# Kernel tuning notes

Hardware: AMD Instinct MI355X
Metric: run time of the kernel (lower is better)

The kernel has to match this reference:

```python
import jax, jax.numpy as jnp
import numpy as np

N = 20000      # nodes
E = 320000     # edges (before self-loops)
G = 64         # graphs in batch
H = 4          # attention heads
C = 64         # channels per head
HID = H * C    # 256
IN = 128       # input feature dim
LAT = 64       # latent dim
NEG = 0.2      # LeakyReLU negative slope (PyG GATConv default)
BN_EPS = 1e-5
N_LAYERS = 3


def setup_inputs() -> dict:
    key = jax.random.key(0)
    ks = jax.random.split(key, 24)
    s = 0.1
    return dict(
        x=jax.random.normal(ks[0], (N, IN), jnp.float32),
        edge_index=jax.random.randint(ks[1], (2, E), 0, N, dtype=jnp.int32),
        batch=jnp.sort(jax.random.randint(ks[2], (N,), 0, G, dtype=jnp.int32)),
        W0=jax.random.normal(ks[3], (IN, HID), jnp.float32) * s,
        W_rest=jax.random.normal(ks[4], (N_LAYERS - 1, HID, HID), jnp.float32) * s,
        att_src=jax.random.normal(ks[5], (N_LAYERS, H, C), jnp.float32) * s,
        att_dst=jax.random.normal(ks[6], (N_LAYERS, H, C), jnp.float32) * s,
        bias_conv=jax.random.normal(ks[7], (N_LAYERS, HID), jnp.float32) * s,
        bn_gamma=jax.random.uniform(ks[8], (N_LAYERS, HID), jnp.float32) + 0.5,
        bn_beta=jax.random.normal(ks[9], (N_LAYERS, HID), jnp.float32) * s,
        bn_mean=jax.random.normal(ks[10], (N_LAYERS, HID), jnp.float32) * s,
        bn_var=jax.random.uniform(ks[11], (N_LAYERS, HID), jnp.float32) + 0.5,
        lbn_gamma=jax.random.uniform(ks[12], (HID,), jnp.float32) + 0.5,
        lbn_beta=jax.random.normal(ks[13], (HID,), jnp.float32) * s,
        lbn_mean=jax.random.normal(ks[14], (HID,), jnp.float32) * s,
        lbn_var=jax.random.uniform(ks[15], (HID,), jnp.float32) + 0.5,
        fc_W=jax.random.normal(ks[16], (HID, LAT), jnp.float32) * s,
        fc_b=jax.random.normal(ks[17], (LAT,), jnp.float32) * s,
    )


def _gat_layer(x, src, dst, W, a_src, a_dst, bias):
    # linear transform -> [N, H, C]
    xp = (x @ W).reshape(N, H, C)
    # per-node attention scalars [N, H]
    al_s = (xp * a_src).sum(-1)
    al_d = (xp * a_dst).sum(-1)
    # per-edge logit for edge j->i: leaky_relu(a_s[j] + a_d[i])
    e = jax.nn.leaky_relu(al_s[src] + al_d[dst], NEG)  # [E', H]
    # softmax over incoming edges of each target node
    emax = jax.ops.segment_max(e, dst, num_segments=N)  # [N, H]
    ex = jnp.exp(e - emax[dst])
    denom = jax.ops.segment_sum(ex, dst, num_segments=N)
    alpha = ex / (denom[dst] + 1e-16)
    # weighted scatter-add of source features
    msg = xp[src] * alpha[:, :, None]                    # [E', H, C]
    out = jax.ops.segment_sum(msg, dst, num_segments=N)  # [N, H, C]
    return out.reshape(N, HID) + bias


def _bn_eval(x, gamma, beta, mean, var):
    return (x - mean) * jax.lax.rsqrt(var + BN_EPS) * gamma + beta


def reference(x, edge_index, batch, W0, W_rest, att_src, att_dst, bias_conv,
              bn_gamma, bn_beta, bn_mean, bn_var,
              lbn_gamma, lbn_beta, lbn_mean, lbn_var, fc_W, fc_b):
    # PyG convention: edge_index[0]=source, edge_index[1]=target; GATConv adds self-loops
    loop = jnp.arange(N, dtype=edge_index.dtype)
    src = jnp.concatenate([edge_index[0], loop])
    dst = jnp.concatenate([edge_index[1], loop])
    h = x
    for i in range(N_LAYERS):
        W = W0 if i == 0 else W_rest[i - 1]
        h = _gat_layer(h, src, dst, W, att_src[i], att_dst[i], bias_conv[i])
        h = _bn_eval(h, bn_gamma[i], bn_beta[i], bn_mean[i], bn_var[i])
        h = jax.nn.relu(h)
        # dropout is identity in eval mode
    pooled = jax.ops.segment_sum(h, batch, num_segments=G)  # [G, HID]
    pooled = _bn_eval(pooled, lbn_gamma, lbn_beta, lbn_mean, lbn_var)
    return pooled @ fc_W + fc_b  # [G, LAT]
```

## Files before the change

### kernel.cpp

```cpp
#include <hip/hip_runtime.h>
#include <hip/hip_bf16.h>
#include <cmath>

#define NN   20000
#define NE   320000
#define EE   (NE + NN)
#define NG   64
#define NH   4
#define NC   64
#define HIDD 256
#define IND  128
#define LATD 64
#define NEGS 0.2f
#define BNEPS 1e-5f
#define MPAD 20096
#define PSPLIT 16

#define BM 128
#define BN 64
#define BK 64

typedef __attribute__((ext_vector_type(8))) short short8;
typedef __attribute__((ext_vector_type(4))) float f32x4;

__device__ inline int lower_bound_i(const int* __restrict__ b, int n, int key) {
    int lo = 0, hi = n;
    while (lo < hi) { int mid = (lo + hi) >> 1; if (b[mid] < key) lo = mid + 1; else hi = mid; }
    return lo;
}

__device__ inline float sel4(float4 v, int h) {
    float r = v.x;
    r = (h == 1) ? v.y : r;
    r = (h == 2) ? v.z : r;
    r = (h == 3) ? v.w : r;
    return r;
}

__device__ inline float bf2f(unsigned short u) {
    return __uint_as_float(((unsigned int)u) << 16);
}

__global__ void k_cast_x(const float* __restrict__ x, __hip_bfloat16* __restrict__ hbx) {
    int i = blockIdx.x * blockDim.x + threadIdx.x;
    if (i >= NN * IND / 4) return;
    float4 v = ((const float4*)x)[i];
    union { __hip_bfloat16 b[4]; ushort4 u; } cv;
    cv.b[0] = __float2bfloat16(v.x); cv.b[1] = __float2bfloat16(v.y);
    cv.b[2] = __float2bfloat16(v.z); cv.b[3] = __float2bfloat16(v.w);
    ((ushort4*)hbx)[i] = cv.u;
}

__global__ void k_cast_wt(const float* __restrict__ W, int K, __hip_bfloat16* __restrict__ Wt) {
    int k = blockIdx.x;
    int n = threadIdx.x;
    Wt[(size_t)n * K + k] = __float2bfloat16(W[(size_t)k * HIDD + n]);
}

__global__ void k_hist(const int* __restrict__ ei, int* __restrict__ deg) {
    int e = blockIdx.x * blockDim.x + threadIdx.x;
    if (e >= EE) return;
    int d = (e < NE) ? ei[NE + e] : (e - NE);
    atomicAdd(&deg[d], 1);
}

#define SCHUNK ((NN + 255) / 256)
__global__ __launch_bounds__(256) void k_scan256(const int* __restrict__ deg,
                                                 int* __restrict__ row_ptr,
                                                 int* __restrict__ cursor) {
    __shared__ int part[256];
    int tid = threadIdx.x;
    int base = tid * SCHUNK;
    int cnt = NN - base; cnt = cnt < 0 ? 0 : (cnt > SCHUNK ? SCHUNK : cnt);
    int sum = 0;
    for (int j = 0; j < cnt; ++j) sum += deg[base + j];
    part[tid] = sum;
    __syncthreads();
    for (int off = 1; off < 256; off <<= 1) {
        int t = (tid >= off) ? part[tid - off] : 0;
        __syncthreads();
        part[tid] += t;
        __syncthreads();
    }
    int excl = part[tid] - sum;
    for (int j = 0; j < cnt; ++j) {
        row_ptr[base + j] = excl; cursor[base + j] = excl;
        excl += deg[base + j];
    }
    if (tid == 255) row_ptr[NN] = part[255];
}

__global__ void k_csr_scatter(const int* __restrict__ ei, int* __restrict__ cursor,
                              int* __restrict__ col_idx) {
    int e = blockIdx.x * blockDim.x + threadIdx.x;
    if (e >= EE) return;
    int s, d;
    if (e < NE) { s = ei[e]; d = ei[NE + e]; } else { s = d = e - NE; }
    int pos = atomicAdd(&cursor[d], 1);
    col_idx[pos] = s;
}

__global__ __launch_bounds__(256) void k_gemm(const short* __restrict__ A,
                                              const short* __restrict__ Bt,
                                              int K, float* __restrict__ C) {
    __shared__ char As[BM * BK * 2];
    __shared__ char Bs[BN * BK * 2];
    int tid = threadIdx.x;
    int lane = tid & 63;
    int wid = tid >> 6;
    int wm = wid >> 1, wn = wid & 1;
    int bm0 = blockIdx.x * BM, bn0 = blockIdx.y * BN;
    int r16 = lane & 15, kg = lane >> 4;

    f32x4 acc[4][2];
    #pragma unroll
    for (int m = 0; m < 4; ++m)
        #pragma unroll
        for (int n = 0; n < 2; ++n) acc[m][n] = (f32x4){0.f, 0.f, 0.f, 0.f};

    for (int k0 = 0; k0 < K; k0 += BK) {
        __syncthreads();
        #pragma unroll
        for (int p = 0; p < 4; ++p) {
            int row = p * 32 + (tid >> 3);
            int cg  = tid & 7;
            uint4 v = *(const uint4*)(A + (size_t)(bm0 + row) * K + k0 + cg * 8);
            *(uint4*)(As + row * 128 + ((cg * 16) ^ ((row & 7) << 4))) = v;
        }
        #pragma unroll
        for (int p = 0; p < 2; ++p) {
            int row = p * 32 + (tid >> 3);
            int cg  = tid & 7;
            uint4 v = *(const uint4*)(Bt + (size_t)(bn0 + row) * K + k0 + cg * 8);
            *(uint4*)(Bs + row * 128 + ((cg * 16) ^ ((row & 7) << 4))) = v;
        }
        __syncthreads();
        #pragma unroll
        for (int kk = 0; kk < 2; ++kk) {
            short8 af[4], bfr[2];
            int kb = (kk * 32 + kg * 8) * 2;
            #pragma unroll
            for (int m = 0; m < 4; ++m) {
                int row = wm * 64 + m * 16 + r16;
                af[m] = *(const short8*)(As + row * 128 + (kb ^ ((row & 7) << 4)));
            }
            #pragma unroll
            for (int n = 0; n < 2; ++n) {
                int row = wn * 32 + n * 16 + r16;
                bfr[n] = *(const short8*)(Bs + row * 128 + (kb ^ ((row & 7) << 4)));
            }
            #pragma unroll
            for (int m = 0; m < 4; ++m)
                #pragma unroll
                for (int n = 0; n < 2; ++n)
                    acc[m][n] = __builtin_amdgcn_mfma_f32_16x16x32_bf16(af[m], bfr[n], acc[m][n], 0, 0, 0);
        }
    }
    #pragma unroll
    for (int m = 0; m < 4; ++m) {
        int row = bm0 + wm * 64 + m * 16 + kg * 4;
        #pragma unroll
        for (int n = 0; n < 2; ++n) {
            int col = bn0 + wn * 32 + n * 16 + r16;
            #pragma unroll
            for (int r = 0; r < 4; ++r)
                C[(size_t)(row + r) * HIDD + col] = acc[m][n][r];
        }
    }
}

__global__ __launch_bounds__(256) void k_att2(const float* __restrict__ xp,
                                              const float* __restrict__ a_src,
                                              const float* __restrict__ a_dst,
                                              float* __restrict__ al_s,
                                              float* __restrict__ al_d,
                                              __hip_bfloat16* __restrict__ xpb) {
    int wid = threadIdx.x >> 6, lane = threadIdx.x & 63;
    int node = blockIdx.x * 4 + wid;
    if (node >= NN) return;
    int hh = lane >> 4, sub = lane & 15;
    float4 v = ((const float4*)(xp + (size_t)node * HIDD))[lane];
    union { __hip_bfloat16 b[4]; ushort4 u; } cv;
    cv.b[0] = __float2bfloat16(v.x); cv.b[1] = __float2bfloat16(v.y);
    cv.b[2] = __float2bfloat16(v.z); cv.b[3] = __float2bfloat16(v.w);
    ((ushort4*)(xpb + (size_t)node * HIDD))[lane] = cv.u;

    float4 ws = ((const float4*)a_src)[lane];
    float4 wd = ((const float4*)a_dst)[lane];
    float s = v.x * ws.x + v.y * ws.y + v.z * ws.z + v.w * ws.w;
    float d = v.x * wd.x + v.y * wd.y + v.z * wd.z + v.w * wd.w;
    #pragma unroll
    for (int m = 1; m < 16; m <<= 1) {
        s += __shfl_xor(s, m, 64);
        d += __shfl_xor(d, m, 64);
    }
    if (sub == 0) {
        al_s[node * NH + hh] = s;
        al_d[node * NH + hh] = d;
    }
}

__global__ __launch_bounds__(256) void k_gat_agg(
        const int* __restrict__ row_ptr, const int* __restrict__ col_idx,
        const float* __restrict__ al_s, const float* __restrict__ al_d,
        const __hip_bfloat16* __restrict__ xpb,
        const float* __restrict__ bias, const float* __restrict__ bg,
        const float* __restrict__ bb, const float* __restrict__ bm,
        const float* __restrict__ bv,
        float* __restrict__ h, __hip_bfloat16* __restrict__ hb, int wmask) {
    int wid = threadIdx.x >> 6, lane = threadIdx.x & 63;
    int node = blockIdx.x * 4 + wid;
    if (node >= NN) return;
    int lo = row_ptr[node], hi = row_ptr[node + 1];
    int hsel = lane >> 4;
    float adh = sel4(((const float4*)al_d)[node], hsel);

    float4 acc0 = {0,0,0,0}, acc1 = {0,0,0,0}, acc2 = {0,0,0,0}, acc3 = {0,0,0,0};
    float den0 = 0.f, den1 = 0.f, den2 = 0.f, den3 = 0.f;

    int e = lo;
    for (; e + 3 < hi; e += 4) {
        int sc0 = col_idx[e], sc1 = col_idx[e + 1], sc2 = col_idx[e + 2], sc3 = col_idx[e + 3];
        float as0 = al_s[sc0 * NH + hsel];
        float as1 = al_s[sc1 * NH + hsel];
        float as2 = al_s[sc2 * NH + hsel];
        float as3 = al_s[sc3 * NH + hsel];
        ushort4 xv0 = ((const ushort4*)(xpb + (size_t)sc0 * HIDD))[lane];
        ushort4 xv1 = ((const ushort4*)(xpb + (size_t)sc1 * HIDD))[lane];
        ushort4 xv2 = ((const ushort4*)(xpb + (size_t)sc2 * HIDD))[lane];
        ushort4 xv3 = ((const ushort4*)(xpb + (size_t)sc3 * HIDD))[lane];
        float l0 = as0 + adh; l0 = l0 > 0.f ? l0 : NEGS * l0;
        float l1 = as1 + adh; l1 = l1 > 0.f ? l1 : NEGS * l1;
        float l2 = as2 + adh; l2 = l2 > 0.f ? l2 : NEGS * l2;
        float l3 = as3 + adh; l3 = l3 > 0.f ? l3 : NEGS * l3;
        float w0 = __expf(l0), w1 = __expf(l1), w2 = __expf(l2), w3 = __expf(l3);
        den0 += w0; den1 += w1; den2 += w2; den3 += w3;
        acc0.x = fmaf(w0, bf2f(xv0.x), acc0.x); acc0.y = fmaf(w0, bf2f(xv0.y), acc0.y);
        acc0.z = fmaf(w0, bf2f(xv0.z), acc0.z); acc0.w = fmaf(w0, bf2f(xv0.w), acc0.w);
        acc1.x = fmaf(w1, bf2f(xv1.x), acc1.x); acc1.y = fmaf(w1, bf2f(xv1.y), acc1.y);
        acc1.z = fmaf(w1, bf2f(xv1.z), acc1.z); acc1.w = fmaf(w1, bf2f(xv1.w), acc1.w);
        acc2.x = fmaf(w2, bf2f(xv2.x), acc2.x); acc2.y = fmaf(w2, bf2f(xv2.y), acc2.y);
        acc2.z = fmaf(w2, bf2f(xv2.z), acc2.z); acc2.w = fmaf(w2, bf2f(xv2.w), acc2.w);
        acc3.x = fmaf(w3, bf2f(xv3.x), acc3.x); acc3.y = fmaf(w3, bf2f(xv3.y), acc3.y);
        acc3.z = fmaf(w3, bf2f(xv3.z), acc3.z); acc3.w = fmaf(w3, bf2f(xv3.w), acc3.w);
    }
    for (; e < hi; ++e) {
        int sc = col_idx[e];
        float as = al_s[sc * NH + hsel];
        ushort4 xv = ((const ushort4*)(xpb + (size_t)sc * HIDD))[lane];
        float l = as + adh; l = l > 0.f ? l : NEGS * l;
        float wt = __expf(l);
        den0 += wt;
        acc0.x = fmaf(wt, bf2f(xv.x), acc0.x); acc0.y = fmaf(wt, bf2f(xv.y), acc0.y);
        acc0.z = fmaf(wt, bf2f(xv.z), acc0.z); acc0.w = fmaf(wt, bf2f(xv.w), acc0.w);
    }

    float inv = 1.f / ((den0 + den1) + (den2 + den3) + 1e-16f);
    float4 acc;
    acc.x = ((acc0.x + acc1.x) + (acc2.x + acc3.x)) * inv;
    acc.y = ((acc0.y + acc1.y) + (acc2.y + acc3.y)) * inv;
    acc.z = ((acc0.z + acc1.z) + (acc2.z + acc3.z)) * inv;
    acc.w = ((acc0.w + acc1.w) + (acc2.w + acc3.w)) * inv;

    float4 bi = ((const float4*)bias)[lane];
    float4 gg = ((const float4*)bg)[lane];
    float4 be = ((const float4*)bb)[lane];
    float4 mn = ((const float4*)bm)[lane];
    float4 vr = ((const float4*)bv)[lane];
    float4 val;
    val.x = (acc.x + bi.x - mn.x) * rsqrtf(vr.x + BNEPS) * gg.x + be.x;
    val.y = (acc.y + bi.y - mn.y) * rsqrtf(vr.y + BNEPS) * gg.y + be.y;
    val.z = (acc.z + bi.z - mn.z) * rsqrtf(vr.z + BNEPS) * gg.z + be.z;
    val.w = (acc.w + bi.w - mn.w) * rsqrtf(vr.w + BNEPS) * gg.w + be.w;
    val.x = val.x > 0.f ? val.x : 0.f;
    val.y = val.y > 0.f ? val.y : 0.f;
    val.z = val.z > 0.f ? val.z : 0.f;
    val.w = val.w > 0.f ? val.w : 0.f;
    if (wmask & 1)
        ((float4*)h)[(size_t)node * 64 + lane] = val;
    if (wmask & 2) {
        union { __hip_bfloat16 b[4]; ushort4 u; } cv;
        cv.b[0] = __float2bfloat16(val.x); cv.b[1] = __float2bfloat16(val.y);
        cv.b[2] = __float2bfloat16(val.z); cv.b[3] = __float2bfloat16(val.w);
        ((ushort4*)hb)[(size_t)node * 64 + lane] = cv.u;
    }
}

__global__ void k_pool2(const float* __restrict__ h, const int* __restrict__ batch,
                        float* __restrict__ partial) {
    int g = blockIdx.x, i = blockIdx.y, col = threadIdx.x;
    int lo = lower_bound_i(batch, NN, g);
    int hi = lower_bound_i(batch, NN, g + 1);
    int len = hi - lo;
    int a = lo + (int)((long)len * i / PSPLIT);
    int b = lo + (int)((long)len * (i + 1) / PSPLIT);
    float acc = 0.f;
    for (int n = a; n < b; ++n) acc += h[(size_t)n * HIDD + col];
    partial[((size_t)g * PSPLIT + i) * HIDD + col] = acc;
}

__global__ __launch_bounds__(64) void k_final(const float* __restrict__ partial,
                                              const float* __restrict__ lg,
                                              const float* __restrict__ lb,
                                              const float* __restrict__ lm,
                                              const float* __restrict__ lv,
                                              const float* __restrict__ fcW,
                                              const float* __restrict__ fcb,
                                              float* __restrict__ out) {
    __shared__ float ps[HIDD];
    int g = blockIdx.x, j = threadIdx.x;
    for (int k = j; k < HIDD; k += 64) {
        float s = 0.f;
        for (int i = 0; i < PSPLIT; ++i)
            s += partial[((size_t)g * PSPLIT + i) * HIDD + k];
        ps[k] = (s - lm[k]) * rsqrtf(lv[k] + BNEPS) * lg[k] + lb[k];
    }
    __syncthreads();
    float acc = 0.f;
    for (int k = 0; k < HIDD; ++k)
        acc = fmaf(ps[k], fcW[k * LATD + j], acc);
    out[g * LATD + j] = acc + fcb[j];
}

extern "C" void kernel_launch(void* const* d_in, const int* in_sizes, int n_in,
                              void* d_out, int out_size, void* d_ws, size_t ws_size,
                              hipStream_t stream) {
    const float* x     = (const float*)d_in[0];
    const int*   ei    = (const int*)d_in[1];
    const int*   batch = (const int*)d_in[2];
    const float* W0    = (const float*)d_in[3];
    const float* Wr    = (const float*)d_in[4];
    const float* asrc  = (const float*)d_in[5];
    const float* adst  = (const float*)d_in[6];
    const float* bconv = (const float*)d_in[7];
    const float* bng   = (const float*)d_in[8];
    const float* bnb   = (const float*)d_in[9];
    const float* bnm   = (const float*)d_in[10];
    const float* bnv   = (const float*)d_in[11];
    const float* lg    = (const float*)d_in[12];
    const float* lb    = (const float*)d_in[13];
    const float* lm    = (const float*)d_in[14];
    const float* lv    = (const float*)d_in[15];
    const float* fcW   = (const float*)d_in[16];
    const float* fcb   = (const float*)d_in[17];
    float* out = (float*)d_out;

    char* w = (char*)d_ws;
    size_t off = 0;
    auto alloc = [&](size_t bytes) {
        char* p = w + off;
        off += (bytes + 255) / 256 * 256;
        return p;
    };
    float* xp    = (float*)alloc((size_t)MPAD * HIDD * 4);
    float* hbuf  = (float*)alloc((size_t)NN * HIDD * 4);
    float* al_s  = (float*)alloc((size_t)NN * NH * 4);
    float* al_d  = (float*)alloc((size_t)NN * NH * 4);
    float* partial = (float*)alloc((size_t)NG * PSPLIT * HIDD * 4);
    __hip_bfloat16* hbx = (__hip_bfloat16*)alloc((size_t)MPAD * IND * 2);
    __hip_bfloat16* hb2 = (__hip_bfloat16*)alloc((size_t)MPAD * HIDD * 2);
    __hip_bfloat16* xpb = (__hip_bfloat16*)alloc((size_t)NN * HIDD * 2);
    __hip_bfloat16* Wt  = (__hip_bfloat16*)alloc((size_t)HIDD * HIDD * 2);
    int* deg     = (int*)alloc((size_t)NN * 4);
    int* row_ptr = (int*)alloc((size_t)(NN + 1) * 4);
    int* cursor  = (int*)alloc((size_t)NN * 4);
    int* col_idx = (int*)alloc((size_t)EE * 4);

    hipMemsetAsync(deg, 0, (size_t)NN * sizeof(int), stream);
    hipLaunchKernelGGL(k_hist, dim3((EE + 255) / 256), dim3(256), 0, stream, ei, deg);
    hipLaunchKernelGGL(k_scan256, dim3(1), dim3(256), 0, stream, deg, row_ptr, cursor);
    hipLaunchKernelGGL(k_csr_scatter, dim3((EE + 255) / 256), dim3(256), 0, stream,
                       ei, cursor, col_idx);

    hipLaunchKernelGGL(k_cast_x, dim3((NN * IND / 4 + 255) / 256), dim3(256), 0, stream, x, hbx);

    for (int layer = 0; layer < 3; ++layer) {
        const float* W = (layer == 0) ? W0 : (Wr + (size_t)(layer - 1) * HIDD * HIDD);
        int K          = (layer == 0) ? IND : HIDD;
        const __hip_bfloat16* Ab = (layer == 0) ? hbx : hb2;
        int wmask      = (layer == 2) ? 1 : 2;

        hipLaunchKernelGGL(k_cast_wt, dim3(K), dim3(HIDD), 0, stream, W, K, Wt);
        hipLaunchKernelGGL(k_gemm, dim3(MPAD / BM, HIDD / BN), dim3(256), 0, stream,
                           (const short*)Ab, (const short*)Wt, K, xp);
        hipLaunchKernelGGL(k_att2, dim3((NN + 3) / 4), dim3(256), 0, stream,
                           xp, asrc + layer * NH * NC, adst + layer * NH * NC, al_s, al_d, xpb);
        hipLaunchKernelGGL(k_gat_agg, dim3((NN + 3) / 4), dim3(256), 0, stream,
                           row_ptr, col_idx, al_s, al_d, xpb,
                           bconv + layer * HIDD, bng + layer * HIDD, bnb + layer * HIDD,
                           bnm + layer * HIDD, bnv + layer * HIDD, hbuf, hb2, wmask);
    }

    hipLaunchKernelGGL(k_pool2, dim3(NG, PSPLIT), dim3(HIDD), 0, stream, hbuf, batch, partial);
    hipLaunchKernelGGL(k_final, dim3(NG), dim3(LATD), 0, stream,
                       partial, lg, lb, lm, lv, fcW, fcb, out);
}
```

Before: 253.8 us.

## Parallelize CSR scan across blocks and emit bf16 directly from GEMM

Replaces the single-block serial degree scan with a three-kernel block-parallel scan (block sums, scan of block sums, apply). The GEMM now writes bf16 output directly instead of fp32, so k_att2 reads the bf16 features and no longer converts and re-stores them. This removes fp32 xp write/read traffic per layer and the serial scan's long latency. In exchange the attention logits are computed from bf16-rounded features rather than fp32, and the scan now takes two extra kernel launches.

```diff
diff --git a/kernel.cpp b/kernel.cpp
--- a/kernel.cpp
+++ b/kernel.cpp
@@ -15,6 +15,7 @@
 #define BNEPS 1e-5f
 #define MPAD 20096
 #define PSPLIT 16
+#define NB   ((NN + 255) / 256)
 
 #define BM 128
 #define BN 64
@@ -64,30 +65,56 @@
     atomicAdd(&deg[d], 1);
 }
 
-#define SCHUNK ((NN + 255) / 256)
-__global__ __launch_bounds__(256) void k_scan256(const int* __restrict__ deg,
-                                                 int* __restrict__ row_ptr,
-                                                 int* __restrict__ cursor) {
-    __shared__ int part[256];
+__global__ __launch_bounds__(256) void k_blocksum(const int* __restrict__ deg,
+                                                  int* __restrict__ bsum) {
+    __shared__ int s[256];
+    int i = blockIdx.x * 256 + threadIdx.x;
+    s[threadIdx.x] = (i < NN) ? deg[i] : 0;
+    __syncthreads();
+    for (int off = 128; off > 0; off >>= 1) {
+        if (threadIdx.x < off) s[threadIdx.x] += s[threadIdx.x + off];
+        __syncthreads();
+    }
+    if (threadIdx.x == 0) bsum[blockIdx.x] = s[0];
+}
+
+__global__ __launch_bounds__(128) void k_scanbs(const int* __restrict__ bsum,
+                                                int* __restrict__ boff,
+                                                int* __restrict__ row_ptr) {
+    __shared__ int s[128];
     int tid = threadIdx.x;
-    int base = tid * SCHUNK;
-    int cnt = NN - base; cnt = cnt < 0 ? 0 : (cnt > SCHUNK ? SCHUNK : cnt);
-    int sum = 0;
-    for (int j = 0; j < cnt; ++j) sum += deg[base + j];
-    part[tid] = sum;
+    int v = (tid < NB) ? bsum[tid] : 0;
+    s[tid] = v;
+    __syncthreads();
+    for (int off = 1; off < 128; off <<= 1) {
+        int t = (tid >= off) ? s[tid - off] : 0;
+        __syncthreads();
+        s[tid] += t;
+        __syncthreads();
+    }
+    if (tid < NB) boff[tid] = s[tid] - v;
+    if (tid == NB - 1) row_ptr[NN] = s[tid];
+}
+
+__global__ __launch_bounds__(256) void k_scanapply(const int* __restrict__ deg,
+                                                   const int* __restrict__ boff,
+                                                   int* __restrict__ row_ptr,
+                                                   int* __restrict__ cursor) {
+    __shared__ int s[256];
+    int i = blockIdx.x * 256 + threadIdx.x;
+    int v = (i < NN) ? deg[i] : 0;
+    s[threadIdx.x] = v;
     __syncthreads();
     for (int off = 1; off < 256; off <<= 1) {
-        int t = (tid >= off) ? part[tid - off] : 0;
-        __syncthreads();
-        part[tid] += t;
-        __syncthreads();
-    }
-    int excl = part[tid] - sum;
-    for (int j = 0; j < cnt; ++j) {
-        row_ptr[base + j] = excl; cursor[base + j] = excl;
-        excl += deg[base + j];
-    }
-    if (tid == 255) row_ptr[NN] = part[255];
+        int t = (threadIdx.x >= off) ? s[threadIdx.x - off] : 0;
+        __syncthreads();
+        s[threadIdx.x] += t;
+        __syncthreads();
+    }
+    if (i < NN) {
+        int excl = boff[blockIdx.x] + s[threadIdx.x] - v;
+        row_ptr[i] = excl; cursor[i] = excl;
+    }
 }
 
 __global__ void k_csr_scatter(const int* __restrict__ ei, int* __restrict__ cursor,
@@ -102,7 +129,7 @@
 
 __global__ __launch_bounds__(256) void k_gemm(const short* __restrict__ A,
                                               const short* __restrict__ Bt,
-                                              int K, float* __restrict__ C) {
+                                              int K, __hip_bfloat16* __restrict__ Cb) {
     __shared__ char As[BM * BK * 2];
     __shared__ char Bs[BN * BK * 2];
     int tid = threadIdx.x;
@@ -164,27 +191,22 @@
             int col = bn0 + wn * 32 + n * 16 + r16;
             #pragma unroll
             for (int r = 0; r < 4; ++r)
-                C[(size_t)(row + r) * HIDD + col] = acc[m][n][r];
+                Cb[(size_t)(row + r) * HIDD + col] = __float2bfloat16(acc[m][n][r]);
         }
     }
 }
 
-__global__ __launch_bounds__(256) void k_att2(const float* __restrict__ xp,
+__global__ __launch_bounds__(256) void k_att2(const __hip_bfloat16* __restrict__ xpb,
                                               const float* __restrict__ a_src,
                                               const float* __restrict__ a_dst,
                                               float* __restrict__ al_s,
-                                              float* __restrict__ al_d,
-                                              __hip_bfloat16* __restrict__ xpb) {
+                                              float* __restrict__ al_d) {
     int wid = threadIdx.x >> 6, lane = threadIdx.x & 63;
     int node = blockIdx.x * 4 + wid;
     if (node >= NN) return;
     int hh = lane >> 4, sub = lane & 15;
-    float4 v = ((const float4*)(xp + (size_t)node * HIDD))[lane];
-    union { __hip_bfloat16 b[4]; ushort4 u; } cv;
-    cv.b[0] = __float2bfloat16(v.x); cv.b[1] = __float2bfloat16(v.y);
-    cv.b[2] = __float2bfloat16(v.z); cv.b[3] = __float2bfloat16(v.w);
-    ((ushort4*)(xpb + (size_t)node * HIDD))[lane] = cv.u;
-
+    ushort4 u = ((const ushort4*)(xpb + (size_t)node * HIDD))[lane];
+    float4 v = {bf2f(u.x), bf2f(u.y), bf2f(u.z), bf2f(u.w)};
     float4 ws = ((const float4*)a_src)[lane];
     float4 wd = ((const float4*)a_dst)[lane];
     float s = v.x * ws.x + v.y * ws.y + v.z * ws.z + v.w * ws.w;
@@ -352,23 +374,26 @@
         off += (bytes + 255) / 256 * 256;
         return p;
     };
-    float* xp    = (float*)alloc((size_t)MPAD * HIDD * 4);
     float* hbuf  = (float*)alloc((size_t)NN * HIDD * 4);
     float* al_s  = (float*)alloc((size_t)NN * NH * 4);
     float* al_d  = (float*)alloc((size_t)NN * NH * 4);
     float* partial = (float*)alloc((size_t)NG * PSPLIT * HIDD * 4);
     __hip_bfloat16* hbx = (__hip_bfloat16*)alloc((size_t)MPAD * IND * 2);
     __hip_bfloat16* hb2 = (__hip_bfloat16*)alloc((size_t)MPAD * HIDD * 2);
-    __hip_bfloat16* xpb = (__hip_bfloat16*)alloc((size_t)NN * HIDD * 2);
+    __hip_bfloat16* xpb = (__hip_bfloat16*)alloc((size_t)MPAD * HIDD * 2);
     __hip_bfloat16* Wt  = (__hip_bfloat16*)alloc((size_t)HIDD * HIDD * 2);
     int* deg     = (int*)alloc((size_t)NN * 4);
     int* row_ptr = (int*)alloc((size_t)(NN + 1) * 4);
     int* cursor  = (int*)alloc((size_t)NN * 4);
     int* col_idx = (int*)alloc((size_t)EE * 4);
+    int* bsum    = (int*)alloc((size_t)NB * 4);
+    int* boff    = (int*)alloc((size_t)NB * 4);
 
     hipMemsetAsync(deg, 0, (size_t)NN * sizeof(int), stream);
     hipLaunchKernelGGL(k_hist, dim3((EE + 255) / 256), dim3(256), 0, stream, ei, deg);
-    hipLaunchKernelGGL(k_scan256, dim3(1), dim3(256), 0, stream, deg, row_ptr, cursor);
+    hipLaunchKernelGGL(k_blocksum, dim3(NB), dim3(256), 0, stream, deg, bsum);
+    hipLaunchKernelGGL(k_scanbs, dim3(1), dim3(128), 0, stream, bsum, boff, row_ptr);
+    hipLaunchKernelGGL(k_scanapply, dim3(NB), dim3(256), 0, stream, deg, boff, row_ptr, cursor);
     hipLaunchKernelGGL(k_csr_scatter, dim3((EE + 255) / 256), dim3(256), 0, stream,
                        ei, cursor, col_idx);
 
@@ -382,9 +407,9 @@
 
         hipLaunchKernelGGL(k_cast_wt, dim3(K), dim3(HIDD), 0, stream, W, K, Wt);
         hipLaunchKernelGGL(k_gemm, dim3(MPAD / BM, HIDD / BN), dim3(256), 0, stream,
-                           (const short*)Ab, (const short*)Wt, K, xp);
+                           (const short*)Ab, (const short*)Wt, K, xpb);
         hipLaunchKernelGGL(k_att2, dim3((NN + 3) / 4), dim3(256), 0, stream,
-                           xp, asrc + layer * NH * NC, adst + layer * NH * NC, al_s, al_d, xpb);
+                           xpb, asrc + layer * NH * NC, adst + layer * NH * NC, al_s, al_d);
         hipLaunchKernelGGL(k_gat_agg, dim3((NN + 3) / 4), dim3(256), 0, stream,
                            row_ptr, col_idx, al_s, al_d, xpb,
                            bconv + layer * HIDD, bng + layer * HIDD, bnb + layer * HIDD,
```

Measured after the change: 205.6 us. -19.0%, faster.
